# Optimization experiments

Measured on AMD Instinct MI355X. Metric: run time of the kernel, lower is better.

The kernel has to match this reference:

```python
import jax, jax.numpy as jnp
import numpy as np

B, T, H, O = 256, 512, 1024, 10


def setup_inputs() -> dict:
    key = jax.random.key(0)
    ks = jax.random.split(key, 6)
    return {
        "x": jax.random.normal(ks[0], (B, T), dtype=jnp.float32),
        "W_hx": jax.random.normal(ks[1], (1, H), dtype=jnp.float32),
        "W_hh": jax.random.normal(ks[2], (H, H), dtype=jnp.float32),
        "W_ph": jax.random.normal(ks[3], (H, O), dtype=jnp.float32),
        "b_h": jax.random.normal(ks[4], (H,), dtype=jnp.float32),
        "b_o": jax.random.normal(ks[5], (O,), dtype=jnp.float32),
    }


def reference(x, W_hx, W_hh, W_ph, b_h, b_o):
    # Precompute input projections for all steps at once: [B,T,1]@[1,H] -> [B,T,H]
    xp = x[:, :, None] * W_hx[None, None, 0, :] + b_h  # [B,T,H]
    h0 = jnp.zeros((x.shape[0], W_hh.shape[0]), dtype=x.dtype)

    def step(h, xp_t):
        h = jnp.tanh(xp_t + h @ W_hh)
        return h, None

    h_final, _ = jax.lax.scan(step, h0, jnp.swapaxes(xp, 0, 1))  # scan over T
    return h_final @ W_ph + b_o
```

## Files before the change

kernel.cpp:

```cpp
#include <hip/hip_runtime.h>
#include <math.h>


#define HH 1024
#define TT 512
#define BB 256
#define OO 10
#define NGRP 8
#define NCT 32
#define NTH 512
#define KH 512

__device__ __forceinline__ float tanh_ref(float x) {
    const float kClamp = 7.99881172180175781f;
    float xc = fminf(fmaxf(x, -kClamp), kClamp);
    float x2 = __fmul_rn(xc, xc);
    float p = -2.76076847742355e-16f;
    p = fmaf(x2, p,  2.00018790482477e-13f);
    p = fmaf(x2, p, -8.60467152213735e-11f);
    p = fmaf(x2, p,  5.12229709037114e-08f);
    p = fmaf(x2, p,  1.48572235717979e-05f);
    p = fmaf(x2, p,  6.37261928875436e-04f);
    p = fmaf(x2, p,  4.89352455891786e-03f);
    p = __fmul_rn(xc, p);
    float q = 1.19825839466702e-06f;
    q = fmaf(x2, q, 1.18534705686654e-04f);
    q = fmaf(x2, q, 2.26843463243900e-03f);
    q = fmaf(x2, q, 4.89352518554385e-03f);
    float r = __fdiv_rn(p, q);
    return (fabsf(x) < 0.0004f) ? x : r;
}

#define MACC(acc, hv, wv) acc = __fadd_rn(acc, __fmul_rn(hv, wv))

#define GROUPSYNC_FAST(target_) {                                                   \
    __syncthreads();                                                                 \
    if (tid == 0) {                                                                  \
        __hip_atomic_fetch_add(&ctr[g], 1, __ATOMIC_RELAXED, __HIP_MEMORY_SCOPE_AGENT); \
        while (__hip_atomic_load(&ctr[g], __ATOMIC_RELAXED, __HIP_MEMORY_SCOPE_AGENT)   \
               < (target_))                                                          \
            __builtin_amdgcn_s_sleep(2);                                             \
    }                                                                                \
    __syncthreads();                                                                 \
    asm volatile("buffer_inv" ::: "memory");                                         \
}

__global__ void __launch_bounds__(NTH, 1) rnn_persist(
    const float* __restrict__ x, const float* __restrict__ Whx,
    const float* __restrict__ Whh, const float* __restrict__ Wph,
    const float* __restrict__ bh, const float* __restrict__ bo,
    float* __restrict__ out, float* __restrict__ ws)
{
    __shared__ float wldsT[32][1024];

    const int bid  = blockIdx.x;
    const int g    = bid & 7;
    const int ct   = bid >> 3;
    const int tid  = threadIdx.x;
    const int w    = tid >> 6;
    const int lane = tid & 63;
    const int c32  = lane & 31;
    const int slot = lane >> 5;
    const int j0   = ct * 32;
    const int j    = j0 + c32;
    const int r0w  = g * 32 + w * 4 + slot * 2;
    const int swz  = (c32 & 7) << 2;

    float* hAbuf = ws;
    float* hBbuf = ws + (BB * HH);
    int*   ctr   = (int*)(ws + 2 * BB * HH);

    const float whx_j = Whx[j];
    const float bh_j  = bh[j];

    #pragma unroll
    for (int i = 0; i < 64; ++i) {
        const int e = tid + i * NTH;
        const int k = e >> 5;
        const int c = e & 31;
        wldsT[c][k ^ ((c & 7) << 2)] = Whh[(size_t)k * HH + j0 + c];
    }

    hAbuf[(size_t)(r0w + 0) * HH + j] = 0.0f;
    hAbuf[(size_t)(r0w + 1) * HH + j] = 0.0f;
    GROUPSYNC_FAST(NCT)

    for (int t = 0; t < TT; ++t) {
        const float* hsrc = (t & 1) ? hBbuf : hAbuf;
        float*       hdst = (t & 1) ? hAbuf : hBbuf;

        const float* h0p = hsrc + (size_t)(r0w + 0) * HH;
        const float* h1p = hsrc + (size_t)(r0w + 1) * HH;
        const float* wrow = wldsT[c32];

        float a0 = 0.f, a1 = 0.f;
        float b0 = 0.f, b1 = 0.f;

        #pragma unroll 2
        for (int k4 = 0; k4 < KH; k4 += 4) {
            const float4 ha0 = *(const float4*)(h0p + k4);
            const float4 ha1 = *(const float4*)(h1p + k4);
            const float4 hb0 = *(const float4*)(h0p + KH + k4);
            const float4 hb1 = *(const float4*)(h1p + KH + k4);
            const float4 w4 = *(const float4*)(wrow + (k4 ^ swz));
            const float4 v4 = *(const float4*)(wrow + ((KH + k4) ^ swz));
            MACC(a0, ha0.x, w4.x); MACC(a1, ha1.x, w4.x);
            MACC(b0, hb0.x, v4.x); MACC(b1, hb1.x, v4.x);
            MACC(a0, ha0.y, w4.y); MACC(a1, ha1.y, w4.y);
            MACC(b0, hb0.y, v4.y); MACC(b1, hb1.y, v4.y);
            MACC(a0, ha0.z, w4.z); MACC(a1, ha1.z, w4.z);
            MACC(b0, hb0.z, v4.z); MACC(b1, hb1.z, v4.z);
            MACC(a0, ha0.w, w4.w); MACC(a1, ha1.w, w4.w);
            MACC(b0, hb0.w, v4.w); MACC(b1, hb1.w, v4.w);
        }

        {
            const float m0 = __fadd_rn(a0, b0);
            const float m1 = __fadd_rn(a1, b1);
            const float xv0 = x[(r0w + 0) * TT + t];
            const float xv1 = x[(r0w + 1) * TT + t];
            hdst[(size_t)(r0w + 0) * HH + j] =
                tanh_ref(__fadd_rn(__fadd_rn(__fmul_rn(xv0, whx_j), bh_j), m0));
            hdst[(size_t)(r0w + 1) * HH + j] =
                tanh_ref(__fadd_rn(__fadd_rn(__fmul_rn(xv1, whx_j), bh_j), m1));
        }

        GROUPSYNC_FAST(NCT * (t + 2))
    }

    if (ct == 0) {
        #pragma unroll 1
        for (int p = w; p < 32 * OO; p += 8) {
            const int rr = p / OO, o = p % OO;
            const int row = g * 32 + rr;
            float v = 0.0f;
            #pragma unroll
            for (int m = 0; m < HH / 64; ++m) {
                const int k = lane + (m << 6);
                v = fmaf(hAbuf[(size_t)row * HH + k], Wph[k * OO + o], v);
            }
            #pragma unroll
            for (int s = 32; s > 0; s >>= 1) v += __shfl_down(v, s, 64);
            if (lane == 0) out[row * OO + o] = v + bo[o];
        }
    }
}

extern "C" void kernel_launch(void* const* d_in, const int* in_sizes, int n_in,
                              void* d_out, int out_size, void* d_ws, size_t ws_size,
                              hipStream_t stream) {
    const float* x   = (const float*)d_in[0];
    const float* Whx = (const float*)d_in[1];
    const float* Whh = (const float*)d_in[2];
    const float* Wph = (const float*)d_in[3];
    const float* bh  = (const float*)d_in[4];
    const float* bo  = (const float*)d_in[5];
    float* out = (float*)d_out;
    float* ws  = (float*)d_ws;

    hipMemsetAsync((char*)d_ws + (size_t)2 * BB * HH * 4, 0, 64, stream);

    void* args[] = {(void*)&x, (void*)&Whx, (void*)&Whh, (void*)&Wph,
                    (void*)&bh, (void*)&bo, (void*)&out, (void*)&ws};
    hipLaunchCooperativeKernel((void*)rnn_persist, dim3(NGRP * NCT), dim3(NTH),
                               args, 0, stream);
}
```

Before: 15.02 ms.

## Double threads per block and remap lanes to one output per thread

Raises the block size from 512 to 1024 threads and gives each thread a single (row, column) output instead of two rows. Lanes are remapped to an 8x8 tile per wavefront, so each wave reads 8 different h rows and 8 LDS weight columns rather than 2 rows and 32 columns. The aim is more waves in flight to hide global h-load and LDS latency in the serial recurrence. In exchange, each weight value pulled from LDS is reused across fewer rows, LDS bank access patterns change, and a 1024-thread block may get fewer registers per thread.

```diff
diff --git a/kernel.cpp b/kernel.cpp
--- a/kernel.cpp
+++ b/kernel.cpp
@@ -8,7 +8,7 @@
 #define OO 10
 #define NGRP 8
 #define NCT 32
-#define NTH 512
+#define NTH 1024
 #define KH 512
 
 __device__ __forceinline__ float tanh_ref(float x) {
@@ -59,11 +59,13 @@
     const int tid  = threadIdx.x;
     const int w    = tid >> 6;
     const int lane = tid & 63;
-    const int c32  = lane & 31;
-    const int slot = lane >> 5;
+    const int c8   = lane & 7;
+    const int r8   = lane >> 3;
+    const int c32  = (w & 3) * 8 + c8;
+    const int row_l= (w >> 2) * 8 + r8;
     const int j0   = ct * 32;
     const int j    = j0 + c32;
-    const int r0w  = g * 32 + w * 4 + slot * 2;
+    const int row  = g * 32 + row_l;
     const int swz  = (c32 & 7) << 2;
 
     float* hAbuf = ws;
@@ -74,55 +76,43 @@
     const float bh_j  = bh[j];
 
     #pragma unroll
-    for (int i = 0; i < 64; ++i) {
+    for (int i = 0; i < 32; ++i) {
         const int e = tid + i * NTH;
         const int k = e >> 5;
         const int c = e & 31;
         wldsT[c][k ^ ((c & 7) << 2)] = Whh[(size_t)k * HH + j0 + c];
     }
 
-    hAbuf[(size_t)(r0w + 0) * HH + j] = 0.0f;
-    hAbuf[(size_t)(r0w + 1) * HH + j] = 0.0f;
+    hAbuf[(size_t)row * HH + j] = 0.0f;
     GROUPSYNC_FAST(NCT)
 
     for (int t = 0; t < TT; ++t) {
         const float* hsrc = (t & 1) ? hBbuf : hAbuf;
         float*       hdst = (t & 1) ? hAbuf : hBbuf;
 
-        const float* h0p = hsrc + (size_t)(r0w + 0) * HH;
-        const float* h1p = hsrc + (size_t)(r0w + 1) * HH;
+        const float* hp = hsrc + (size_t)row * HH;
         const float* wrow = wldsT[c32];
 
-        float a0 = 0.f, a1 = 0.f;
-        float b0 = 0.f, b1 = 0.f;
+        float a = 0.f;
+        float b = 0.f;
 
-        #pragma unroll 2
+        #pragma unroll 4
         for (int k4 = 0; k4 < KH; k4 += 4) {
-            const float4 ha0 = *(const float4*)(h0p + k4);
-            const float4 ha1 = *(const float4*)(h1p + k4);
-            const float4 hb0 = *(const float4*)(h0p + KH + k4);
-            const float4 hb1 = *(const float4*)(h1p + KH + k4);
+            const float4 ha = *(const float4*)(hp + k4);
+            const float4 hb = *(const float4*)(hp + KH + k4);
             const float4 w4 = *(const float4*)(wrow + (k4 ^ swz));
             const float4 v4 = *(const float4*)(wrow + ((KH + k4) ^ swz));
-            MACC(a0, ha0.x, w4.x); MACC(a1, ha1.x, w4.x);
-            MACC(b0, hb0.x, v4.x); MACC(b1, hb1.x, v4.x);
-            MACC(a0, ha0.y, w4.y); MACC(a1, ha1.y, w4.y);
-            MACC(b0, hb0.y, v4.y); MACC(b1, hb1.y, v4.y);
-            MACC(a0, ha0.z, w4.z); MACC(a1, ha1.z, w4.z);
-            MACC(b0, hb0.z, v4.z); MACC(b1, hb1.z, v4.z);
-            MACC(a0, ha0.w, w4.w); MACC(a1, ha1.w, w4.w);
-            MACC(b0, hb0.w, v4.w); MACC(b1, hb1.w, v4.w);
+            MACC(a, ha.x, w4.x); MACC(b, hb.x, v4.x);
+            MACC(a, ha.y, w4.y); MACC(b, hb.y, v4.y);
+            MACC(a, ha.z, w4.z); MACC(b, hb.z, v4.z);
+            MACC(a, ha.w, w4.w); MACC(b, hb.w, v4.w);
         }
 
         {
-            const float m0 = __fadd_rn(a0, b0);
-            const float m1 = __fadd_rn(a1, b1);
-            const float xv0 = x[(r0w + 0) * TT + t];
-            const float xv1 = x[(r0w + 1) * TT + t];
-            hdst[(size_t)(r0w + 0) * HH + j] =
-                tanh_ref(__fadd_rn(__fadd_rn(__fmul_rn(xv0, whx_j), bh_j), m0));
-            hdst[(size_t)(r0w + 1) * HH + j] =
-                tanh_ref(__fadd_rn(__fadd_rn(__fmul_rn(xv1, whx_j), bh_j), m1));
+            const float m = __fadd_rn(a, b);
+            const float xv = x[(size_t)row * TT + t];
+            hdst[(size_t)row * HH + j] =
+                tanh_ref(__fadd_rn(__fadd_rn(__fmul_rn(xv, whx_j), bh_j), m));
         }
 
         GROUPSYNC_FAST(NCT * (t + 2))
@@ -130,18 +120,18 @@
 
     if (ct == 0) {
         #pragma unroll 1
-        for (int p = w; p < 32 * OO; p += 8) {
+        for (int p = w; p < 32 * OO; p += 16) {
             const int rr = p / OO, o = p % OO;
-            const int row = g * 32 + rr;
+            const int orow = g * 32 + rr;
             float v = 0.0f;
             #pragma unroll
             for (int m = 0; m < HH / 64; ++m) {
                 const int k = lane + (m << 6);
-                v = fmaf(hAbuf[(size_t)row * HH + k], Wph[k * OO + o], v);
+                v = fmaf(hAbuf[(size_t)orow * HH + k], Wph[k * OO + o], v);
             }
             #pragma unroll
             for (int s = 32; s > 0; s >>= 1) v += __shfl_down(v, s, 64);
-            if (lane == 0) out[row * OO + o] = v + bo[o];
+            if (lane == 0) out[orow * OO + o] = v + bo[o];
         }
     }
 }
```

New measurement: 15.04 ms (median of 2 runs). No clear change (+0.1%).
